# Optimization experiments

Measured on AMD Instinct MI355X. Metric: run time of the kernel, lower is better.

Reference implementation:

```python
import jax, jax.numpy as jnp
import numpy as np

B, C, N_MAX = 32, 1, 1024
HID, CLS, ATT_E, ATT_H = 128, 64, 64, 128
D = HID + CLS            # node_state_dim = hidden + class_repr
EDGE_F = 2 * ATT_E       # 128
K_MIX = 20
N_GNN = B * C * N_MAX    # 32768 GNN nodes
N_FEAT = N_GNN + 1       # node_feat rows after zero-pad row
E = 200_000
E_OUT = 500_000
NUM_SUB = 1024
NUM_PROP = 2             # num_GNN_prop (num_GNN_layers = 1)


def _lin(k, din, dout):
    k1, k2 = jax.random.split(k)
    s = 1.0 / np.sqrt(din)
    return (jax.random.uniform(k1, (din, dout), minval=-s, maxval=s),
            jax.random.uniform(k2, (dout,), minval=-s, maxval=s))


def setup_inputs() -> dict:
    key = jax.random.key(0)
    ks = jax.random.split(key, 30)
    inp = {}
    inp['A_pad'] = (jax.random.uniform(ks[0], (B, C, N_MAX, N_MAX)) < 0.05).astype(jnp.float32)
    inp['edges'] = jax.random.randint(ks[1], (E, 2), 0, N_GNN)
    inp['att_idx'] = jax.random.randint(ks[2], (N_GNN,), 0, ATT_E)
    inp['node_idx_feat'] = jax.random.randint(ks[3], (N_GNN,), 0, N_FEAT)
    inp['class_label'] = jax.random.randint(ks[4], (N_GNN,), 0, 2)
    inp['node_idx_gnn'] = jax.random.randint(ks[5], (E_OUT, 2), 0, N_GNN)
    inp['label'] = (jax.random.uniform(ks[6], (E_OUT,)) < 0.3).astype(jnp.float32)
    inp['subgraph_idx'] = jax.random.randint(ks[7], (E_OUT,), 0, NUM_SUB)
    # learned parameters
    inp['W_dec'], inp['b_dec'] = _lin(ks[8], N_MAX, HID)
    inp['class_emb'] = jax.random.normal(ks[9], (2, CLS)) * 0.1
    inp['W_msg1'], inp['b_msg1'] = _lin(ks[10], D + EDGE_F, D)
    inp['W_msg2'], inp['b_msg2'] = _lin(ks[11], D, D)
    inp['W_att1'], inp['b_att1'] = _lin(ks[12], D + EDGE_F, ATT_H)
    inp['W_att2'], inp['b_att2'] = _lin(ks[13], ATT_H, D)
    inp['W_ih'], inp['b_ih'] = _lin(ks[14], D, 3 * D)
    inp['W_hh'], inp['b_hh'] = _lin(ks[15], D, 3 * D)
    inp['Wt1'], inp['bt1'] = _lin(ks[16], D, HID)
    inp['Wt2'], inp['bt2'] = _lin(ks[17], HID, HID)
    inp['Wt3'], inp['bt3'] = _lin(ks[18], HID, K_MIX)
    inp['Wa1'], inp['ba1'] = _lin(ks[19], D, HID)
    inp['Wa2'], inp['ba2'] = _lin(ks[20], HID, HID)
    inp['Wa3'], inp['ba3'] = _lin(ks[21], HID, K_MIX)
    return inp


def _gran_forward(A_pad, label, W_dec, b_dec, class_emb,
                  W_msg1, b_msg1, W_msg2, b_msg2, W_att1, b_att1, W_att2, b_att2,
                  W_ih, b_ih, W_hh, b_hh, Wt1, bt1, Wt2, bt2, Wt3, bt3,
                  Wa1, ba1, Wa2, ba2, Wa3, ba3,
                  edges, att_idx, node_idx_feat, class_label, node_idx_gnn, subgraph_idx):
    # decoder_input: (B*C*N_max, N_max) -> hidden, then zero-pad one row on top
    A = A_pad.reshape(B * C * N_MAX, N_MAX)
    node_feat = A @ W_dec + b_dec                                   # [N_GNN, HID]
    node_feat = jnp.concatenate([jnp.zeros((1, HID), node_feat.dtype), node_feat], axis=0)
    # att_edge_feat: one-hot(att_idx[src]) || one-hot(att_idx[dst])  (scatter of ones)
    att_edge_feat = jnp.concatenate([
        jax.nn.one_hot(att_idx[edges[:, 0]], ATT_E, dtype=node_feat.dtype),
        jax.nn.one_hot(att_idx[edges[:, 1]], ATT_E, dtype=node_feat.dtype)], axis=1)  # [E, 128]
    # node state = gathered feat ++ class representation
    state = jnp.concatenate([node_feat[node_idx_feat], class_emb[class_label]], axis=1)  # [N_GNN, D]

    src, dst = edges[:, 0], edges[:, 1]

    def prop(state):
        diff = state[src] - state[dst]                              # gather node-diff [E, D]
        ei = jnp.concatenate([diff, att_edge_feat], axis=1)          # [E, D+128]
        msg = jax.nn.relu(ei @ W_msg1 + b_msg1) @ W_msg2 + b_msg2   # edge MLP [E, D]
        att = jax.nn.sigmoid(jax.nn.relu(ei @ W_att1 + b_att1) @ W_att2 + b_att2)
        agg = jax.ops.segment_sum(msg * att, dst, num_segments=N_GNN)  # scatter-add [N_GNN, D]
        # GRUCell(agg, state)
        gi = agg @ W_ih + b_ih
        gh = state @ W_hh + b_hh
        ir, iz, inn = jnp.split(gi, 3, axis=1)
        hr, hz, hn = jnp.split(gh, 3, axis=1)
        r = jax.nn.sigmoid(ir + hr)
        z = jax.nn.sigmoid(iz + hz)
        n = jnp.tanh(inn + r * hn)
        return (1.0 - z) * n + z * state

    for _ in range(NUM_PROP):
        state = prop(state)

    # output edge predictions from state diffs
    dout = state[node_idx_gnn[:, 0]] - state[node_idx_gnn[:, 1]]    # [E_OUT, D]
    h = jax.nn.relu(jax.nn.relu(dout @ Wt1 + bt1) @ Wt2 + bt2)
    log_theta = h @ Wt3 + bt3                                        # [E_OUT, K]
    g = jax.nn.relu(jax.nn.relu(dout @ Wa1 + ba1) @ Wa2 + ba2)
    log_alpha = jax.nn.log_softmax(g @ Wa3 + ba3, axis=1)            # [E_OUT, K]

    # mixture Bernoulli loss (BCEWithLogits, pos_weight=1): softplus(x) - x*y
    adj_loss = jax.nn.softplus(log_theta) - log_theta * label[:, None]
    const = jax.ops.segment_sum(jnp.ones((E_OUT,), log_theta.dtype), subgraph_idx, num_segments=NUM_SUB)
    const = jnp.maximum(const, 1.0)  # guard empty subgraphs with random indices
    red_loss = jax.ops.segment_sum(adj_loss, subgraph_idx, num_segments=NUM_SUB)
    red_alpha = jax.ops.segment_sum(log_alpha, subgraph_idx, num_segments=NUM_SUB) / const[:, None]
    log_prob = jax.nn.logsumexp(-red_loss + red_alpha, axis=1)       # [NUM_SUB]
    return -jnp.sum(log_prob) / float(E_OUT)


def reference(A_pad, edges, att_idx, node_idx_feat, class_label, node_idx_gnn, label, subgraph_idx,
              W_dec, b_dec, class_emb, W_msg1, b_msg1, W_msg2, b_msg2,
              W_att1, b_att1, W_att2, b_att2, W_ih, b_ih, W_hh, b_hh,
              Wt1, bt1, Wt2, bt2, Wt3, bt3, Wa1, ba1, Wa2, ba2, Wa3, ba3):
    return _gran_forward(A_pad, label, W_dec, b_dec, class_emb,
                         W_msg1, b_msg1, W_msg2, b_msg2, W_att1, b_att1, W_att2, b_att2,
                         W_ih, b_ih, W_hh, b_hh, Wt1, bt1, Wt2, bt2, Wt3, bt3,
                         Wa1, ba1, Wa2, ba2, Wa3, ba3,
                         edges, att_idx, node_idx_feat, class_label, node_idx_gnn, subgraph_idx)
```

## Files before the change

kernel.cpp:

```cpp
#include <hip/hip_runtime.h>
#include <math.h>

#define NGNN   32768
#define NMAXD  1024
#define HIDD   128
#define CLSD   64
#define DDIM   192
#define ATTH   128
#define NEDGE  200000
#define NEOUT  500000
#define NSUB   1024
#define KMIX   20

#define NREP      64
#define LOSS_OFF  0
#define ALPHA_OFF 20480
#define CNT_OFF   40960
#define REP_STRIDE 41984

typedef __attribute__((ext_vector_type(8))) short bf16x8;
typedef __attribute__((ext_vector_type(8))) unsigned short u16x8;
typedef __attribute__((ext_vector_type(4))) float f32x4;

__device__ __forceinline__ float sigm(float x) { return 1.0f / (1.0f + __expf(-x)); }
__device__ __forceinline__ float tanhf_(float x) { return 2.0f / (1.0f + __expf(-2.0f * x)) - 1.0f; }

__device__ __forceinline__ short f2bf(float f) {
  union { float f; unsigned u; } v; v.f = f;
  unsigned r = v.u + 0x7FFFu + ((v.u >> 16) & 1u);
  return (short)(r >> 16);
}
__device__ __forceinline__ float bf2f(unsigned short u) {
  union { unsigned u; float f; } v; v.u = ((unsigned)u) << 16;
  return v.f;
}
__device__ __forceinline__ f32x4 bc4(float b) {
  f32x4 v; v[0] = b; v[1] = b; v[2] = b; v[3] = b; return v;
}

__global__ __launch_bounds__(64) void k_pack(const float* __restrict__ W,
                                             short* __restrict__ out, int N, int CT) {
  const int l = threadIdx.x;
  const int ks = blockIdx.x / CT;
  const int ct = blockIdx.x % CT;
  const int row0 = ks * 32 + (l >> 4) * 8;
  const int col = ct * 16 + (l & 15);
  short v[8];
#pragma unroll
  for (int j = 0; j < 8; j++) {
    const float f = (col < N) ? W[(size_t)(row0 + j) * N + col] : 0.0f;
    v[j] = f2bf(f);
  }
  *(bf16x8*)(out + ((size_t)blockIdx.x * 64 + l) * 8) = *(bf16x8*)v;
}

__global__ __launch_bounds__(128) void k_dec(
    const float* __restrict__ A, const float* __restrict__ Wd,
    const float* __restrict__ bd, float* __restrict__ nf) {
  __shared__ float arow[NMAXD];
  __shared__ int   nz[NMAXD];
  __shared__ int   cnt;
  const int row = blockIdx.x;
  const int t = threadIdx.x;
  if (t == 0) cnt = 0;
  const float4* A4 = (const float4*)(A + (size_t)row * NMAXD);
  float4* a4 = (float4*)arow;
  a4[t] = A4[t];
  a4[t + 128] = A4[t + 128];
  __syncthreads();
  for (int i = t; i < NMAXD; i += 128) {
    if (arow[i] != 0.0f) {
      int p = atomicAdd(&cnt, 1);
      nz[p] = i;
    }
  }
  __syncthreads();
  float acc = bd[t];
  const int n = cnt;
  for (int i = 0; i < n; i++) acc += Wd[(size_t)nz[i] * HIDD + t];
  nf[(size_t)row * HIDD + t] = acc;
}

__global__ __launch_bounds__(192) void k_state(
    const float* __restrict__ nf, const float* __restrict__ cemb,
    const int* __restrict__ nif, const int* __restrict__ cl,
    unsigned short* __restrict__ stbf) {
  const int i = blockIdx.x;
  const int t = threadIdx.x;
  float v;
  if (t < HIDD) {
    const int idx = nif[i];
    v = (idx == 0) ? 0.0f : nf[(size_t)(idx - 1) * HIDD + t];
  } else {
    v = cemb[cl[i] * CLSD + (t - HIDD)];
  }
  stbf[(size_t)i * DDIM + t] = (unsigned short)f2bf(v);
}

__global__ __launch_bounds__(256, 2) void k_edge_mfma(
    const unsigned short* __restrict__ stbf, const int* __restrict__ edges,
    const int* __restrict__ attidx,
    const float* __restrict__ bm1,
    const short* __restrict__ pWm1, const short* __restrict__ pWm2,
    const float* __restrict__ bm2,
    const float* __restrict__ ba1,
    const short* __restrict__ pWa1, const short* __restrict__ pWa2,
    const float* __restrict__ ba2,
    float* __restrict__ agg) {
  __shared__ short pdiff[12288];
  __shared__ short phm[12288];
  __shared__ short pha[8192];
  __shared__ int   sa0[64], sa1[64], sdst[64];

  const int t = threadIdx.x;
  const int e0 = blockIdx.x * 64;
  const int wid = t >> 6, l = t & 63;
  const int col16 = l & 15, rr = (l >> 4) * 4;
  const int cb = (l >> 4) * 8;

  if (t < 64) {
    const int s = edges[2 * (e0 + t)];
    const int d = edges[2 * (e0 + t) + 1];
    sa0[t] = attidx[s] + 192;
    sa1[t] = attidx[d] + 256;
    sdst[t] = d;
  }
  for (int it = 0; it < 6; it++) {
    const int id = t + 256 * it;
    const int r = id / 24, g24 = id % 24;
    const int e = e0 + r;
    const int s = edges[2 * e], d = edges[2 * e + 1];
    const u16x8 a = *(const u16x8*)&stbf[(size_t)s * DDIM + g24 * 8];
    const u16x8 b = *(const u16x8*)&stbf[(size_t)d * DDIM + g24 * 8];
    short v[8];
#pragma unroll
    for (int j = 0; j < 8; j++) v[j] = f2bf(bf2f(a[j]) - bf2f(b[j]));
    const int rt = r >> 4, ks = g24 >> 2, g = g24 & 3;
    *(bf16x8*)&pdiff[((rt * 6 + ks) * 64 + g * 16 + (r & 15)) * 8] = *(bf16x8*)v;
  }
  __syncthreads();

  int a0v[4], a1v[4];
#pragma unroll
  for (int rt = 0; rt < 4; rt++) {
    a0v[rt] = sa0[rt * 16 + (l & 15)];
    a1v[rt] = sa1[rt * 16 + (l & 15)];
  }

  const int w5 = wid * 5;

  {
    f32x4 acc[5][4];
#pragma unroll
    for (int u = 0; u < 5; u++)
#pragma unroll
      for (int rt = 0; rt < 4; rt++) acc[u][rt] = bc4(0.0f);

    for (int ks = 0; ks < 10; ks++) {
      bf16x8 A[4];
      if (ks < 6) {
#pragma unroll
        for (int rt = 0; rt < 4; rt++)
          A[rt] = *(const bf16x8*)&pdiff[((rt * 6 + ks) * 64 + l) * 8];
      } else {
        const int kb = ks * 32 + cb;
#pragma unroll
        for (int rt = 0; rt < 4; rt++) {
          short v[8];
#pragma unroll
          for (int j = 0; j < 8; j++) {
            const int kg = kb + j;
            v[j] = (kg == a0v[rt] || kg == a1v[rt]) ? (short)0x3F80 : (short)0;
          }
          A[rt] = *(bf16x8*)v;
        }
      }
      bf16x8 B[5];
#pragma unroll
      for (int u = 0; u < 5; u++) {
        const int unit = w5 + u;
        const short* bp = (unit < 12)
            ? &pWm1[((ks * 12 + unit) * 64 + l) * 8]
            : &pWa1[((ks * 8 + (unit - 12)) * 64 + l) * 8];
        B[u] = *(const bf16x8*)bp;
      }
#pragma unroll
      for (int u = 0; u < 5; u++)
#pragma unroll
        for (int rt = 0; rt < 4; rt++)
          acc[u][rt] = __builtin_amdgcn_mfma_f32_16x16x32_bf16(A[rt], B[u], acc[u][rt], 0, 0, 0);
    }

#pragma unroll
    for (int u = 0; u < 5; u++) {
      const int unit = w5 + u;
      const int isMsg = (unit < 12);
      const int ct = isMsg ? unit : unit - 12;
      const int col = ct * 16 + col16;
      const float bb = isMsg ? bm1[col] : ba1[col];
      const int ksp = col >> 5, gp = (col & 31) >> 3, jp = col & 7;
#pragma unroll
      for (int rt = 0; rt < 4; rt++)
#pragma unroll
        for (int j = 0; j < 4; j++) {
          const short hv = f2bf(fmaxf(acc[u][rt][j] + bb, 0.0f));
          if (isMsg) phm[((rt * 6 + ksp) * 64 + gp * 16 + rr + j) * 8 + jp] = hv;
          else       pha[((rt * 4 + ksp) * 64 + gp * 16 + rr + j) * 8 + jp] = hv;
        }
    }
  }
  __syncthreads();

  {
    const int w3 = wid * 3;
    f32x4 m[3][4], av[3][4];
#pragma unroll
    for (int c = 0; c < 3; c++) {
      const int col = (w3 + c) * 16 + col16;
      const f32x4 bm = bc4(bm2[col]), ba = bc4(ba2[col]);
#pragma unroll
      for (int rt = 0; rt < 4; rt++) { m[c][rt] = bm; av[c][rt] = ba; }
    }
    for (int ks = 0; ks < 6; ks++) {
      bf16x8 A[4];
#pragma unroll
      for (int rt = 0; rt < 4; rt++)
        A[rt] = *(const bf16x8*)&phm[((rt * 6 + ks) * 64 + l) * 8];
      bf16x8 B[3];
#pragma unroll
      for (int c = 0; c < 3; c++)
        B[c] = *(const bf16x8*)&pWm2[((ks * 12 + w3 + c) * 64 + l) * 8];
#pragma unroll
      for (int c = 0; c < 3; c++)
#pragma unroll
        for (int rt = 0; rt < 4; rt++)
          m[c][rt] = __builtin_amdgcn_mfma_f32_16x16x32_bf16(A[rt], B[c], m[c][rt], 0, 0, 0);
    }
    for (int ks = 0; ks < 4; ks++) {
      bf16x8 A[4];
#pragma unroll
      for (int rt = 0; rt < 4; rt++)
        A[rt] = *(const bf16x8*)&pha[((rt * 4 + ks) * 64 + l) * 8];
      bf16x8 B[3];
#pragma unroll
      for (int c = 0; c < 3; c++)
        B[c] = *(const bf16x8*)&pWa2[((ks * 12 + w3 + c) * 64 + l) * 8];
#pragma unroll
      for (int c = 0; c < 3; c++)
#pragma unroll
        for (int rt = 0; rt < 4; rt++)
          av[c][rt] = __builtin_amdgcn_mfma_f32_16x16x32_bf16(A[rt], B[c], av[c][rt], 0, 0, 0);
    }
#pragma unroll
    for (int c = 0; c < 3; c++) {
      const int col = (w3 + c) * 16 + col16;
#pragma unroll
      for (int rt = 0; rt < 4; rt++)
#pragma unroll
        for (int j = 0; j < 4; j++) {
          const int dst = sdst[rt * 16 + rr + j];
          atomicAdd(&agg[(size_t)dst * DDIM + col], m[c][rt][j] * sigm(av[c][rt][j]));
        }
    }
  }
}

__global__ __launch_bounds__(256, 2) void k_gru_mfma(
    unsigned short* __restrict__ stbf, const float* __restrict__ agg,
    const short* __restrict__ pWih, const float* __restrict__ bih,
    const short* __restrict__ pWhh, const float* __restrict__ bhh) {
  const int t = threadIdx.x;
  const int n0 = blockIdx.x * 64;
  const int wid = t >> 6, l = t & 63;
  const int col16 = l & 15, rr = (l >> 4) * 4;
  const int cb = (l >> 4) * 8;
  const int row = n0 + wid * 16 + (l & 15);

  bf16x8 af[6], sf[6];
#pragma unroll
  for (int ks = 0; ks < 6; ks++) {
    const float4 a0 = *(const float4*)&agg[(size_t)row * DDIM + ks * 32 + cb];
    const float4 a1 = *(const float4*)&agg[(size_t)row * DDIM + ks * 32 + cb + 4];
    short v[8];
    v[0] = f2bf(a0.x); v[1] = f2bf(a0.y); v[2] = f2bf(a0.z); v[3] = f2bf(a0.w);
    v[4] = f2bf(a1.x); v[5] = f2bf(a1.y); v[6] = f2bf(a1.z); v[7] = f2bf(a1.w);
    af[ks] = *(bf16x8*)v;
    sf[ks] = *(const bf16x8*)&stbf[(size_t)row * DDIM + ks * 32 + cb];
  }

  for (int ct = 0; ct < 12; ct++) {
    const int c = ct * 16 + col16;
    f32x4 ir = bc4(bih[c]), iz = bc4(bih[c + DDIM]), in_ = bc4(bih[c + 2 * DDIM]);
    f32x4 hr = bc4(bhh[c]), hz = bc4(bhh[c + DDIM]), hn = bc4(bhh[c + 2 * DDIM]);
#pragma unroll
    for (int ks = 0; ks < 6; ks++) {
      const bf16x8 wr = *(const bf16x8*)&pWih[((size_t)(ks * 36 + ct) * 64 + l) * 8];
      const bf16x8 wz = *(const bf16x8*)&pWih[((size_t)(ks * 36 + ct + 12) * 64 + l) * 8];
      const bf16x8 wn = *(const bf16x8*)&pWih[((size_t)(ks * 36 + ct + 24) * 64 + l) * 8];
      ir  = __builtin_amdgcn_mfma_f32_16x16x32_bf16(af[ks], wr, ir, 0, 0, 0);
      iz  = __builtin_amdgcn_mfma_f32_16x16x32_bf16(af[ks], wz, iz, 0, 0, 0);
      in_ = __builtin_amdgcn_mfma_f32_16x16x32_bf16(af[ks], wn, in_, 0, 0, 0);
      const bf16x8 vr = *(const bf16x8*)&pWhh[((size_t)(ks * 36 + ct) * 64 + l) * 8];
      const bf16x8 vz = *(const bf16x8*)&pWhh[((size_t)(ks * 36 + ct + 12) * 64 + l) * 8];
      const bf16x8 vn = *(const bf16x8*)&pWhh[((size_t)(ks * 36 + ct + 24) * 64 + l) * 8];
      hr = __builtin_amdgcn_mfma_f32_16x16x32_bf16(sf[ks], vr, hr, 0, 0, 0);
      hz = __builtin_amdgcn_mfma_f32_16x16x32_bf16(sf[ks], vz, hz, 0, 0, 0);
      hn = __builtin_amdgcn_mfma_f32_16x16x32_bf16(sf[ks], vn, hn, 0, 0, 0);
    }
#pragma unroll
    for (int j = 0; j < 4; j++) {
      const size_t idx = (size_t)(n0 + wid * 16 + rr + j) * DDIM + c;
      const float sv = bf2f(stbf[idx]);
      const float r = sigm(ir[j] + hr[j]);
      const float z = sigm(iz[j] + hz[j]);
      const float nn = tanhf_(in_[j] + r * hn[j]);
      stbf[idx] = (unsigned short)f2bf((1.0f - z) * nn + z * sv);
    }
  }
}

__global__ __launch_bounds__(512, 4) void k_head_mfma(
    const unsigned short* __restrict__ stbf, const int* __restrict__ nig,
    const float* __restrict__ label, const int* __restrict__ subidx,
    const short* __restrict__ pWt1, const float* __restrict__ bt1,
    const short* __restrict__ pWt2, const float* __restrict__ bt2,
    const short* __restrict__ pWt3, const float* __restrict__ bt3,
    const short* __restrict__ pWa1, const float* __restrict__ ba1,
    const short* __restrict__ pWa2, const float* __restrict__ ba2,
    const short* __restrict__ pWa3, const float* __restrict__ ba3,
    float* __restrict__ REP) {
  __shared__ short u1[16384];
  __shared__ short ph1[16384];
  __shared__ float la[64 * KMIX];
  __shared__ int   ssub[64];
  __shared__ float slab[64];
  __shared__ float lse[64];

  const int t = threadIdx.x;
  const int r0 = blockIdx.x * 64;
  float* rep = REP + (size_t)(blockIdx.x & (NREP - 1)) * REP_STRIDE;

  if (t < 64) {
    const int gr = r0 + t;
    const int sb = (gr < NEOUT) ? subidx[gr] : 0;
    ssub[t] = sb;
    slab[t] = (gr < NEOUT) ? label[gr] : 0.0f;
    if (gr < NEOUT) atomicAdd(&rep[CNT_OFF + sb], 1.0f);
  }

  for (int it = 0; it < 3; it++) {
    const int id = t + 512 * it;
    const int r = id / 24, g24 = id % 24;
    const int gr = r0 + r;
    const int ok = (gr < NEOUT);
    const int ia = ok ? nig[2 * gr] : 0;
    const int ib = ok ? nig[2 * gr + 1] : 0;
    const u16x8 a = *(const u16x8*)&stbf[(size_t)ia * DDIM + g24 * 8];
    const u16x8 b = *(const u16x8*)&stbf[(size_t)ib * DDIM + g24 * 8];
    short v[8];
#pragma unroll
    for (int j = 0; j < 8; j++) v[j] = f2bf(bf2f(a[j]) - bf2f(b[j]));
    const int rt = r >> 4, ks = g24 >> 2, g = g24 & 3;
    *(bf16x8*)&u1[((rt * 6 + ks) * 64 + g * 16 + (r & 15)) * 8] = *(bf16x8*)v;
  }
  __syncthreads();

  const int wid = t >> 6, l = t & 63;
  const int b = wid >> 2, cw = wid & 3;
  const int col16 = l & 15, rr = (l >> 4) * 4;

  const short* pW1 = b ? pWa1 : pWt1;
  const short* pW2 = b ? pWa2 : pWt2;
  const short* pW3 = b ? pWa3 : pWt3;
  const float* bv1 = b ? ba1 : bt1;
  const float* bv2 = b ? ba2 : bt2;
  const float* bv3 = b ? ba3 : bt3;
  short* ph1b = ph1 + b * 8192;
  short* ph2b = u1 + b * 8192;

  {
    bf16x8 B1[12];
    float bias[2];
#pragma unroll
    for (int c2 = 0; c2 < 2; c2++) {
      const int ct = cw * 2 + c2;
      bias[c2] = bv1[ct * 16 + col16];
#pragma unroll
      for (int ks = 0; ks < 6; ks++)
        B1[c2 * 6 + ks] = *(const bf16x8*)&pW1[((ks * 8 + ct) * 64 + l) * 8];
    }
    for (int rt = 0; rt < 4; rt++) {
      bf16x8 a[6];
#pragma unroll
      for (int ks = 0; ks < 6; ks++)
        a[ks] = *(const bf16x8*)&u1[((rt * 6 + ks) * 64 + l) * 8];
      f32x4 acc0 = bc4(bias[0]), acc1 = bc4(bias[1]);
#pragma unroll
      for (int ks = 0; ks < 6; ks++) {
        acc0 = __builtin_amdgcn_mfma_f32_16x16x32_bf16(a[ks], B1[ks], acc0, 0, 0, 0);
        acc1 = __builtin_amdgcn_mfma_f32_16x16x32_bf16(a[ks], B1[6 + ks], acc1, 0, 0, 0);
      }
#pragma unroll
      for (int c2 = 0; c2 < 2; c2++) {
        const int col = (cw * 2 + c2) * 16 + col16;
        const int ksp = col >> 5, gp = (col & 31) >> 3, jp = col & 7;
        const f32x4 acc = c2 ? acc1 : acc0;
#pragma unroll
        for (int j = 0; j < 4; j++)
          ph1b[((rt * 4 + ksp) * 64 + gp * 16 + rr + j) * 8 + jp] = f2bf(fmaxf(acc[j], 0.0f));
      }
    }
  }
  __syncthreads();

  {
    bf16x8 B2[8];
    float bias[2];
#pragma unroll
    for (int c2 = 0; c2 < 2; c2++) {
      const int ct = cw * 2 + c2;
      bias[c2] = bv2[ct * 16 + col16];
#pragma unroll
      for (int ks = 0; ks < 4; ks++)
        B2[c2 * 4 + ks] = *(const bf16x8*)&pW2[((ks * 8 + ct) * 64 + l) * 8];
    }
    for (int rt = 0; rt < 4; rt++) {
      bf16x8 a[4];
#pragma unroll
      for (int ks = 0; ks < 4; ks++)
        a[ks] = *(const bf16x8*)&ph1b[((rt * 4 + ks) * 64 + l) * 8];
      f32x4 acc0 = bc4(bias[0]), acc1 = bc4(bias[1]);
#pragma unroll
      for (int ks = 0; ks < 4; ks++) {
        acc0 = __builtin_amdgcn_mfma_f32_16x16x32_bf16(a[ks], B2[ks], acc0, 0, 0, 0);
        acc1 = __builtin_amdgcn_mfma_f32_16x16x32_bf16(a[ks], B2[4 + ks], acc1, 0, 0, 0);
      }
#pragma unroll
      for (int c2 = 0; c2 < 2; c2++) {
        const int col = (cw * 2 + c2) * 16 + col16;
        const int ksp = col >> 5, gp = (col & 31) >> 3, jp = col & 7;
        const f32x4 acc = c2 ? acc1 : acc0;
#pragma unroll
        for (int j = 0; j < 4; j++)
          ph2b[((rt * 4 + ksp) * 64 + gp * 16 + rr + j) * 8 + jp] = f2bf(fmaxf(acc[j], 0.0f));
      }
    }
  }
  __syncthreads();

  {
    const int ct3 = cw & 1, rth = cw >> 1;
    const int col = ct3 * 16 + col16;
    bf16x8 B3[4];
#pragma unroll
    for (int ks = 0; ks < 4; ks++)
      B3[ks] = *(const bf16x8*)&pW3[((ks * 2 + ct3) * 64 + l) * 8];
    const float bias = (col < KMIX) ? bv3[col] : 0.0f;
#pragma unroll
    for (int i = 0; i < 2; i++) {
      const int rt = rth * 2 + i;
      bf16x8 a[4];
#pragma unroll
      for (int ks = 0; ks < 4; ks++)
        a[ks] = *(const bf16x8*)&ph2b[((rt * 4 + ks) * 64 + l) * 8];
      f32x4 acc = bc4(bias);
#pragma unroll
      for (int ks = 0; ks < 4; ks++)
        acc = __builtin_amdgcn_mfma_f32_16x16x32_bf16(a[ks], B3[ks], acc, 0, 0, 0);
      if (col < KMIX) {
        if (b == 0) {
#pragma unroll
          for (int j = 0; j < 4; j++) {
            const int r = rt * 16 + rr + j;
            if (r0 + r < NEOUT) {
              const float lt = acc[j];
              const float adj = fmaxf(lt, 0.0f) + logf(1.0f + __expf(-fabsf(lt))) - lt * slab[r];
              atomicAdd(&rep[LOSS_OFF + ssub[r] * KMIX + col], adj);
            }
          }
        } else {
#pragma unroll
          for (int j = 0; j < 4; j++)
            la[(rt * 16 + rr + j) * KMIX + col] = acc[j];
        }
      }
    }
  }
  __syncthreads();
  if (t < 64) {
    float m = -1e30f;
    for (int k = 0; k < KMIX; k++) m = fmaxf(m, la[t * KMIX + k]);
    float s = 0.0f;
    for (int k = 0; k < KMIX; k++) s += __expf(la[t * KMIX + k] - m);
    lse[t] = m + logf(s);
  }
  __syncthreads();
  {
    const int r = t >> 3;
    if (r0 + r < NEOUT) {
#pragma unroll
      for (int i = 0; i < 3; i++) {
        const int c = (t & 7) + 8 * i;
        if (c < KMIX)
          atomicAdd(&rep[ALPHA_OFF + ssub[r] * KMIX + c], la[r * KMIX + c] - lse[r]);
      }
    }
  }
}

__global__ __launch_bounds__(256) void k_red(const float* __restrict__ REP,
                                             float* __restrict__ fin) {
  const int i = blockIdx.x * 256 + threadIdx.x;
  if (i < REP_STRIDE) {
    float s = 0.0f;
    for (int r = 0; r < NREP; r++) s += REP[(size_t)r * REP_STRIDE + i];
    fin[i] = s;
  }
}

__global__ __launch_bounds__(1024) void k_final(
    const float* __restrict__ fin, float* __restrict__ out) {
  __shared__ float part[1024];
  const int s = threadIdx.x;
  const float* red_loss  = fin + LOSS_OFF;
  const float* red_alpha = fin + ALPHA_OFF;
  const float c = fmaxf(fin[CNT_OFF + s], 1.0f);
  float v[KMIX];
  float m = -1e30f;
  for (int k = 0; k < KMIX; k++) {
    v[k] = -red_loss[s * KMIX + k] + red_alpha[s * KMIX + k] / c;
    m = fmaxf(m, v[k]);
  }
  float sum = 0.0f;
  for (int k = 0; k < KMIX; k++) sum += __expf(v[k] - m);
  part[s] = m + logf(sum);
  __syncthreads();
  for (int st = 512; st > 0; st >>= 1) {
    if (s < st) part[s] += part[s + st];
    __syncthreads();
  }
  if (s == 0) out[0] = -part[0] / (float)NEOUT;
}

extern "C" void kernel_launch(void* const* d_in, const int* in_sizes, int n_in,
                              void* d_out, int out_size, void* d_ws, size_t ws_size,
                              hipStream_t stream) {
  const float* A      = (const float*)d_in[0];
  const int*   edges  = (const int*)d_in[1];
  const int*   attidx = (const int*)d_in[2];
  const int*   nif    = (const int*)d_in[3];
  const int*   cl     = (const int*)d_in[4];
  const int*   nig    = (const int*)d_in[5];
  const float* label  = (const float*)d_in[6];
  const int*   subidx = (const int*)d_in[7];
  const float* Wdec   = (const float*)d_in[8];
  const float* bdec   = (const float*)d_in[9];
  const float* cemb   = (const float*)d_in[10];
  const float* Wm1    = (const float*)d_in[11];
  const float* bm1    = (const float*)d_in[12];
  const float* Wm2    = (const float*)d_in[13];
  const float* bm2    = (const float*)d_in[14];
  const float* Wa1    = (const float*)d_in[15];
  const float* ba1    = (const float*)d_in[16];
  const float* Wa2    = (const float*)d_in[17];
  const float* ba2    = (const float*)d_in[18];
  const float* Wih    = (const float*)d_in[19];
  const float* bih    = (const float*)d_in[20];
  const float* Whh    = (const float*)d_in[21];
  const float* bhh    = (const float*)d_in[22];
  const float* Wt1    = (const float*)d_in[23];
  const float* bt1    = (const float*)d_in[24];
  const float* Wt2    = (const float*)d_in[25];
  const float* bt2    = (const float*)d_in[26];
  const float* Wt3    = (const float*)d_in[27];
  const float* bt3    = (const float*)d_in[28];
  const float* Wha1   = (const float*)d_in[29];
  const float* hba1   = (const float*)d_in[30];
  const float* Wha2   = (const float*)d_in[31];
  const float* hba2   = (const float*)d_in[32];
  const float* Wha3   = (const float*)d_in[33];
  const float* hba3   = (const float*)d_in[34];

  char* ws = (char*)d_ws;
  const size_t SZ_STBF = (size_t)NGNN * DDIM * sizeof(short);
  const size_t SZ_AGG  = (size_t)NGNN * DDIM * sizeof(float);
  const size_t SZ_REP  = (size_t)NREP * REP_STRIDE * sizeof(float);
  unsigned short* stbf = (unsigned short*)ws;
  float* agg       = (float*)(ws + SZ_STBF);
  float* nf        = agg;
  float* REP       = (float*)(ws + SZ_STBF + SZ_AGG);
  float* fin       = (float*)(ws + SZ_STBF + SZ_AGG + SZ_REP);
  short* pk        = (short*)(ws + SZ_STBF + SZ_AGG + SZ_REP +
                              (((size_t)REP_STRIDE * 4 + 255) / 256) * 256);
  short* pWm1  = pk;
  short* pWa1e = pWm1  + 61440;
  short* pWm2  = pWa1e + 40960;
  short* pWa2e = pWm2  + 36864;
  short* pWt1  = pWa2e + 24576;
  short* pWt2  = pWt1  + 24576;
  short* pWt3  = pWt2  + 16384;
  short* pWh1  = pWt3  + 4096;
  short* pWh2  = pWh1  + 24576;
  short* pWh3  = pWh2  + 16384;
  short* pWih  = pWh3  + 4096;
  short* pWhh  = pWih  + 110592;

  k_pack<<<120, 64, 0, stream>>>(Wm1,  pWm1,  192, 12);
  k_pack<<< 80, 64, 0, stream>>>(Wa1,  pWa1e, 128, 8);
  k_pack<<< 72, 64, 0, stream>>>(Wm2,  pWm2,  192, 12);
  k_pack<<< 48, 64, 0, stream>>>(Wa2,  pWa2e, 192, 12);
  k_pack<<< 48, 64, 0, stream>>>(Wt1,  pWt1,  128, 8);
  k_pack<<< 32, 64, 0, stream>>>(Wt2,  pWt2,  128, 8);
  k_pack<<<  8, 64, 0, stream>>>(Wt3,  pWt3,   20, 2);
  k_pack<<< 48, 64, 0, stream>>>(Wha1, pWh1,  128, 8);
  k_pack<<< 32, 64, 0, stream>>>(Wha2, pWh2,  128, 8);
  k_pack<<<  8, 64, 0, stream>>>(Wha3, pWh3,   20, 2);
  k_pack<<<216, 64, 0, stream>>>(Wih,  pWih,  576, 36);
  k_pack<<<216, 64, 0, stream>>>(Whh,  pWhh,  576, 36);

  k_dec<<<NGNN, 128, 0, stream>>>(A, Wdec, bdec, nf);
  k_state<<<NGNN, 192, 0, stream>>>(nf, cemb, nif, cl, stbf);
  for (int p = 0; p < 2; p++) {
    hipMemsetAsync(agg, 0, SZ_AGG, stream);
    k_edge_mfma<<<NEDGE / 64, 256, 0, stream>>>(stbf, edges, attidx,
        bm1, pWm1, pWm2, bm2, ba1, pWa1e, pWa2e, ba2, agg);
    k_gru_mfma<<<NGNN / 64, 256, 0, stream>>>(stbf, agg, pWih, bih, pWhh, bhh);
  }
  hipMemsetAsync(REP, 0, SZ_REP, stream);
  k_head_mfma<<<(NEOUT + 63) / 64, 512, 0, stream>>>(stbf, nig, label, subidx,
      pWt1, bt1, pWt2, bt2, pWt3, bt3, pWh1, hba1, pWh2, hba2, pWh3, hba3, REP);
  k_red<<<(REP_STRIDE + 255) / 256, 256, 0, stream>>>(REP, fin);
  k_final<<<1, 1024, 0, stream>>>(fin, (float*)d_out);
}
```

Baseline: 884.9 us.

## Replace atomic edge scatter with CSR gather of bf16 messages in GRU

Builds a CSR index of edges grouped by destination node using a histogram, a scan and a scatter. The edge kernel now writes per-edge gated messages as bf16 into a message buffer staged through shared memory, and the GRU kernel gathers and sums each node's incoming messages. This removes the float atomics into the aggregate buffer and its per-layer memset, at the cost of extra preprocessing kernels, an edge-sized message buffer, and bf16 rounding of each message before summation. Summation order also changes with the nondeterministic scatter order.

Measured after the change: 863.4 us. 1.02x faster.

```diff
diff --git a/kernel.cpp b/kernel.cpp
--- a/kernel.cpp
+++ b/kernel.cpp
@@ -36,6 +36,50 @@
 }
 __device__ __forceinline__ f32x4 bc4(float b) {
   f32x4 v; v[0] = b; v[1] = b; v[2] = b; v[3] = b; return v;
+}
+
+__global__ __launch_bounds__(256) void k_hist(const int* __restrict__ edges,
+                                              int* __restrict__ deg) {
+  const int e = blockIdx.x * 256 + threadIdx.x;
+  if (e < NEDGE) atomicAdd(&deg[edges[2 * e + 1]], 1);
+}
+
+__global__ __launch_bounds__(1024) void k_scan(const int* deg_in,
+                                               int* rowptr, int* cursor) {
+  __shared__ int part[1024];
+  const int t = threadIdx.x;
+  const int base = t * 32;
+  int loc[32];
+  int s = 0;
+#pragma unroll
+  for (int i = 0; i < 32; i++) { loc[i] = deg_in[base + i]; s += loc[i]; }
+  part[t] = s;
+  __syncthreads();
+  for (int off = 1; off < 1024; off <<= 1) {
+    int v = 0;
+    if (t >= off) v = part[t - off];
+    __syncthreads();
+    part[t] += v;
+    __syncthreads();
+  }
+  int pre = (t == 0) ? 0 : part[t - 1];
+#pragma unroll
+  for (int i = 0; i < 32; i++) {
+    rowptr[base + i] = pre;
+    cursor[base + i] = pre;
+    pre += loc[i];
+  }
+  if (t == 1023) rowptr[NGNN] = pre;
+}
+
+__global__ __launch_bounds__(256) void k_scatter(const int* __restrict__ edges,
+                                                 int* __restrict__ cursor,
+                                                 int* __restrict__ eidx) {
+  const int e = blockIdx.x * 256 + threadIdx.x;
+  if (e < NEDGE) {
+    const int p = atomicAdd(&cursor[edges[2 * e + 1]], 1);
+    eidx[p] = e;
+  }
 }
 
 __global__ __launch_bounds__(64) void k_pack(const float* __restrict__ W,
@@ -106,11 +150,11 @@
     const float* __restrict__ ba1,
     const short* __restrict__ pWa1, const short* __restrict__ pWa2,
     const float* __restrict__ ba2,
-    float* __restrict__ agg) {
+    unsigned short* __restrict__ msgbuf) {
   __shared__ short pdiff[12288];
   __shared__ short phm[12288];
   __shared__ short pha[8192];
-  __shared__ int   sa0[64], sa1[64], sdst[64];
+  __shared__ int   sa0[64], sa1[64];
 
   const int t = threadIdx.x;
   const int e0 = blockIdx.x * 64;
@@ -123,7 +167,6 @@
     const int d = edges[2 * (e0 + t) + 1];
     sa0[t] = attidx[s] + 192;
     sa1[t] = attidx[d] + 256;
-    sdst[t] = d;
   }
   for (int it = 0; it < 6; it++) {
     const int id = t + 256 * it;
@@ -251,22 +294,35 @@
         for (int rt = 0; rt < 4; rt++)
           av[c][rt] = __builtin_amdgcn_mfma_f32_16x16x32_bf16(A[rt], B[c], av[c][rt], 0, 0, 0);
     }
+
+    short* msgrow = pdiff;
 #pragma unroll
     for (int c = 0; c < 3; c++) {
       const int col = (w3 + c) * 16 + col16;
 #pragma unroll
       for (int rt = 0; rt < 4; rt++)
 #pragma unroll
-        for (int j = 0; j < 4; j++) {
-          const int dst = sdst[rt * 16 + rr + j];
-          atomicAdd(&agg[(size_t)dst * DDIM + col], m[c][rt][j] * sigm(av[c][rt][j]));
-        }
+        for (int j = 0; j < 4; j++)
+          msgrow[(rt * 16 + rr + j) * DDIM + col] = f2bf(m[c][rt][j] * sigm(av[c][rt][j]));
+    }
+  }
+  __syncthreads();
+
+  {
+    const short* msgrow = pdiff;
+    for (int it = 0; it < 6; it++) {
+      const int id = t + 256 * it;
+      const int r = id / 24, g = id % 24;
+      *(float4*)&msgbuf[(size_t)(e0 + r) * DDIM + g * 8] =
+          *(const float4*)&msgrow[r * DDIM + g * 8];
     }
   }
 }
 
 __global__ __launch_bounds__(256, 2) void k_gru_mfma(
-    unsigned short* __restrict__ stbf, const float* __restrict__ agg,
+    unsigned short* __restrict__ stbf,
+    const unsigned short* __restrict__ msgbuf,
+    const int* __restrict__ rowptr, const int* __restrict__ eidx,
     const short* __restrict__ pWih, const float* __restrict__ bih,
     const short* __restrict__ pWhh, const float* __restrict__ bhh) {
   const int t = threadIdx.x;
@@ -276,14 +332,30 @@
   const int cb = (l >> 4) * 8;
   const int row = n0 + wid * 16 + (l & 15);
 
+  float afacc[6][8];
+#pragma unroll
+  for (int ks = 0; ks < 6; ks++)
+#pragma unroll
+    for (int j = 0; j < 8; j++) afacc[ks][j] = 0.0f;
+
+  const int rbeg = rowptr[row], rend = rowptr[row + 1];
+  for (int p = rbeg; p < rend; p++) {
+    const int e = eidx[p];
+    const unsigned short* mr = &msgbuf[(size_t)e * DDIM + cb];
+#pragma unroll
+    for (int ks = 0; ks < 6; ks++) {
+      const u16x8 cc = *(const u16x8*)(mr + ks * 32);
+#pragma unroll
+      for (int j = 0; j < 8; j++) afacc[ks][j] += bf2f(cc[j]);
+    }
+  }
+
   bf16x8 af[6], sf[6];
 #pragma unroll
   for (int ks = 0; ks < 6; ks++) {
-    const float4 a0 = *(const float4*)&agg[(size_t)row * DDIM + ks * 32 + cb];
-    const float4 a1 = *(const float4*)&agg[(size_t)row * DDIM + ks * 32 + cb + 4];
     short v[8];
-    v[0] = f2bf(a0.x); v[1] = f2bf(a0.y); v[2] = f2bf(a0.z); v[3] = f2bf(a0.w);
-    v[4] = f2bf(a1.x); v[5] = f2bf(a1.y); v[6] = f2bf(a1.z); v[7] = f2bf(a1.w);
+#pragma unroll
+    for (int j = 0; j < 8; j++) v[j] = f2bf(afacc[ks][j]);
     af[ks] = *(bf16x8*)v;
     sf[ks] = *(const bf16x8*)&stbf[(size_t)row * DDIM + ks * 32 + cb];
   }
@@ -583,15 +655,20 @@
 
   char* ws = (char*)d_ws;
   const size_t SZ_STBF = (size_t)NGNN * DDIM * sizeof(short);
-  const size_t SZ_AGG  = (size_t)NGNN * DDIM * sizeof(float);
+  const size_t SZ_MSG  = (size_t)NEDGE * DDIM * sizeof(short);
   const size_t SZ_REP  = (size_t)NREP * REP_STRIDE * sizeof(float);
-  unsigned short* stbf = (unsigned short*)ws;
-  float* agg       = (float*)(ws + SZ_STBF);
-  float* nf        = agg;
-  float* REP       = (float*)(ws + SZ_STBF + SZ_AGG);
-  float* fin       = (float*)(ws + SZ_STBF + SZ_AGG + SZ_REP);
-  short* pk        = (short*)(ws + SZ_STBF + SZ_AGG + SZ_REP +
-                              (((size_t)REP_STRIDE * 4 + 255) / 256) * 256);
+
+  unsigned short* stbf   = (unsigned short*)ws;
+  unsigned short* msgbuf = (unsigned short*)(ws + SZ_STBF);
+  float* nf  = (float*)(ws + SZ_STBF);
+  float* REP = (float*)(ws + SZ_STBF);
+  float* fin = (float*)(ws + SZ_STBF + SZ_REP);
+
+  char* tail = ws + SZ_STBF + SZ_MSG;
+  int* rowptr = (int*)tail;
+  int* degcur = (int*)(tail + 131328);
+  int* eidx   = (int*)(tail + 131328 + 131072);
+  short* pk   = (short*)(tail + 131328 + 131072 + 800000);
   short* pWm1  = pk;
   short* pWa1e = pWm1  + 61440;
   short* pWm2  = pWa1e + 40960;
@@ -605,6 +682,11 @@
   short* pWih  = pWh3  + 4096;
   short* pWhh  = pWih  + 110592;
 
+  hipMemsetAsync(degcur, 0, (size_t)NGNN * sizeof(int), stream);
+  k_hist<<<(NEDGE + 255) / 256, 256, 0, stream>>>(edges, degcur);
+  k_scan<<<1, 1024, 0, stream>>>(degcur, rowptr, degcur);
+  k_scatter<<<(NEDGE + 255) / 256, 256, 0, stream>>>(edges, degcur, eidx);
+
   k_pack<<<120, 64, 0, stream>>>(Wm1,  pWm1,  192, 12);
   k_pack<<< 80, 64, 0, stream>>>(Wa1,  pWa1e, 128, 8);
   k_pack<<< 72, 64, 0, stream>>>(Wm2,  pWm2,  192, 12);
@@ -621,10 +703,10 @@
   k_dec<<<NGNN, 128, 0, stream>>>(A, Wdec, bdec, nf);
   k_state<<<NGNN, 192, 0, stream>>>(nf, cemb, nif, cl, stbf);
   for (int p = 0; p < 2; p++) {
-    hipMemsetAsync(agg, 0, SZ_AGG, stream);
     k_edge_mfma<<<NEDGE / 64, 256, 0, stream>>>(stbf, edges, attidx,
-        bm1, pWm1, pWm2, bm2, ba1, pWa1e, pWa2e, ba2, agg);
-    k_gru_mfma<<<NGNN / 64, 256, 0, stream>>>(stbf, agg, pWih, bih, pWhh, bhh);
+        bm1, pWm1, pWm2, bm2, ba1, pWa1e, pWa2e, ba2, msgbuf);
+    k_gru_mfma<<<NGNN / 64, 256, 0, stream>>>(stbf, msgbuf, rowptr, eidx,
+        pWih, bih, pWhh, bhh);
   }
   hipMemsetAsync(REP, 0, SZ_REP, stream);
   k_head_mfma<<<(NEOUT + 63) / 64, 512, 0, stream>>>(stbf, nig, label, subidx,
```
